# Optimization experiments

Hardware: AMD Instinct MI355X
Metric: run time of the kernel (lower is better)

The kernel has to match this reference:

```python
import jax, jax.numpy as jnp
import numpy as np

N_NODES = 50000
NODE_DIM = 128
HIDDEN = 256
BLOCK_OUT = 128
NUM_CLASSES = 40
N_EDGES = 800000


def setup_inputs() -> dict:
    key = jax.random.key(0)
    ks = jax.random.split(key, 12)
    glorot = lambda k, fi, fo: jax.random.normal(k, (fi, fo), jnp.float32) * (2.0 / (fi + fo)) ** 0.5
    return {
        "x": jax.random.normal(ks[0], (N_NODES, NODE_DIM), jnp.float32),
        "edge_index": jax.random.randint(ks[1], (2, N_EDGES), 0, N_NODES, jnp.int64),
        # block1: Node2Edge MLP (2*node_dim -> hidden), Edge2Node MLP (hidden -> 128)
        "W1": glorot(ks[2], 2 * NODE_DIM, HIDDEN),
        "b1": jnp.zeros((HIDDEN,), jnp.float32),
        "W2": glorot(ks[3], HIDDEN, BLOCK_OUT),
        "b2": jnp.zeros((BLOCK_OUT,), jnp.float32),
        # final Node2Edge: Linear(2*128,128) -> ReLU -> Linear(128,num_classes) -> LogSoftmax
        "W3": glorot(ks[4], 2 * BLOCK_OUT, 128),
        "b3": jnp.zeros((128,), jnp.float32),
        "W4": glorot(ks[5], 128, NUM_CLASSES),
        "b4": jnp.zeros((NUM_CLASSES,), jnp.float32),
    }


def reference(x, edge_index, W1, b1, W2, b2, W3, b3, W4, b4):
    src, dst = edge_index[0], edge_index[1]
    # Node2Edge: gather endpoints, concat, edge MLP
    e = jnp.concatenate([x[src], x[dst]], axis=-1)          # [E, 2*node_dim]
    eh = jax.nn.relu(e @ W1 + b1)                            # [E, hidden]
    # Edge2Node: scatter-mean edge features to destination nodes
    agg = jax.ops.segment_sum(eh, dst, num_segments=N_NODES)
    cnt = jax.ops.segment_sum(jnp.ones((eh.shape[0],), eh.dtype), dst, num_segments=N_NODES)
    mean = agg / jnp.maximum(cnt, 1.0)[:, None]              # [N, hidden]
    h = jax.nn.relu(mean @ W2 + b2)                          # [N, 128]
    # final Node2Edge head -> per-edge class log-probs
    e2 = jnp.concatenate([h[src], h[dst]], axis=-1)          # [E, 256]
    z = jax.nn.relu(e2 @ W3 + b3)                            # [E, 128]
    logits = z @ W4 + b4                                     # [E, num_classes]
    return jax.nn.log_softmax(logits, axis=-1)
```

## Files before the change

### kernel.cpp

```cpp
#include <hip/hip_runtime.h>
#include <hip/hip_bf16.h>


typedef short bf16x8 __attribute__((ext_vector_type(8)));
typedef float f32x4 __attribute__((ext_vector_type(4)));

#define N_NODES 50000
#define N_EDGES 800000

__device__ __forceinline__ unsigned short f2bf(float f) {
  unsigned u = __builtin_bit_cast(unsigned, f);
  u = u + 0x7fffu + ((u >> 16) & 1u);
  return (unsigned short)(u >> 16);
}
__device__ __forceinline__ float bf2f(unsigned short h) {
  unsigned u = ((unsigned)h) << 16;
  return __builtin_bit_cast(float, u);
}
__device__ __forceinline__ int ld_src(const int* ei, int m64, int e) {
  return m64 ? ei[2 * e] : ei[e];
}
__device__ __forceinline__ int ld_dst(const int* ei, int m64, int e) {
  return m64 ? ei[2 * N_EDGES + 2 * e] : ei[N_EDGES + e];
}

__global__ void k_prep_frags(const float* __restrict__ W1, const float* __restrict__ W2,
                             const float* __restrict__ W3, const float* __restrict__ W4,
                             const float* __restrict__ b4,
                             unsigned short* __restrict__ w1f, unsigned short* __restrict__ w2f,
                             unsigned short* __restrict__ w3f, unsigned short* __restrict__ w4f,
                             float* __restrict__ b4p, int* __restrict__ flagp,
                             const int* __restrict__ ei) {
  int gid = blockIdx.x * 256 + threadIdx.x;
  if (gid < 65536) {
    int i = gid & 7, lane = (gid >> 3) & 63, ks = (gid >> 9) & 3, ct = gid >> 11;
    int k = ks * 32 + (lane >> 4) * 8 + i;
    int c = ct * 16 + (lane & 15);
    float v = (c < 256) ? W1[k * 256 + c] : W1[(128 + k) * 256 + (c - 256)];
    w1f[gid] = f2bf(v);
  } else if (gid < 98304) {
    int f = gid - 65536;
    int i = f & 7, lane = (f >> 3) & 63, ks = (f >> 9) & 7, ct = f >> 12;
    int k = ks * 32 + (lane >> 4) * 8 + i;
    int c = ct * 16 + (lane & 15);
    w2f[f] = f2bf(W2[k * 128 + c]);
  } else if (gid < 131072) {
    int f = gid - 98304;
    int i = f & 7, lane = (f >> 3) & 63, ks = (f >> 9) & 3, ct = f >> 11;
    int k = ks * 32 + (lane >> 4) * 8 + i;
    int c = ct * 16 + (lane & 15);
    float v = (c < 128) ? W3[k * 128 + c] : W3[(128 + k) * 128 + (c - 128)];
    w3f[f] = f2bf(v);
  } else if (gid < 137216) {
    int f = gid - 131072;
    int i = f & 7, lane = (f >> 3) & 63, ks = (f >> 9) & 3, ct = f >> 11;
    int k = ks * 32 + (lane >> 4) * 8 + i;
    int c = ct * 16 + (lane & 15);
    w4f[f] = (c < 40) ? f2bf(W4[k * 40 + c]) : (unsigned short)0;
  } else if (gid < 137264) {
    int c = gid - 137216;
    b4p[c] = (c < 40) ? b4[c] : 0.f;
  } else if (gid == 137264) {
    *flagp = (ei[1] == 0 && ei[3] == 0 && ei[5] == 0 && ei[7] == 0) ? 1 : 0;
  }
}

__global__ void k_hist(const int* __restrict__ ei, const int* __restrict__ flagp,
                       int* __restrict__ hist) {
  int e = blockIdx.x * 256 + threadIdx.x;
  atomicAdd(&hist[ld_dst(ei, *flagp, e)], 1);
}

__global__ __launch_bounds__(256) void k_scan_a(const int* __restrict__ hist,
                                                int* __restrict__ bsum) {
  __shared__ int ps[256];
  int t = threadIdx.x, idx = blockIdx.x * 256 + t;
  ps[t] = (idx < N_NODES) ? hist[idx] : 0;
  __syncthreads();
  for (int off = 128; off > 0; off >>= 1) {
    if (t < off) ps[t] += ps[t + off];
    __syncthreads();
  }
  if (t == 0) bsum[blockIdx.x] = ps[0];
}

__global__ __launch_bounds__(256) void k_scan_b(int* __restrict__ bsum, int* __restrict__ seg) {
  __shared__ int ps[256];
  int t = threadIdx.x;
  int v = (t < 196) ? bsum[t] : 0;
  ps[t] = v;
  __syncthreads();
  for (int off = 1; off < 256; off <<= 1) {
    int u = (t >= off) ? ps[t - off] : 0;
    __syncthreads();
    ps[t] += u;
    __syncthreads();
  }
  if (t < 196) bsum[t] = ps[t] - v;
  if (t == 195) seg[N_NODES] = ps[195];
}

__global__ __launch_bounds__(256) void k_scan_c(int* __restrict__ hist,
                                                const int* __restrict__ bsum,
                                                int* __restrict__ seg) {
  __shared__ int ps[256];
  int t = threadIdx.x, idx = blockIdx.x * 256 + t;
  int v = (idx < N_NODES) ? hist[idx] : 0;
  ps[t] = v;
  __syncthreads();
  for (int off = 1; off < 256; off <<= 1) {
    int u = (t >= off) ? ps[t - off] : 0;
    __syncthreads();
    ps[t] += u;
    __syncthreads();
  }
  int run = bsum[blockIdx.x] + ps[t] - v;
  if (idx < N_NODES) {
    seg[idx] = run;
    hist[idx] = run;
  }
}

__global__ void k_scatter(const int* __restrict__ ei, const int* __restrict__ flagp,
                          int* __restrict__ cursor, int* __restrict__ ssrc) {
  int e = blockIdx.x * 256 + threadIdx.x;
  int m64 = *flagp;
  int s = ld_src(ei, m64, e), d = ld_dst(ei, m64, e);
  int pos = atomicAdd(&cursor[d], 1);
  ssrc[pos] = s;
}

__global__ __launch_bounds__(512, 2) void k_sy(const float* __restrict__ x,
                                               const unsigned short* __restrict__ w1f,
                                               const float* __restrict__ b1,
                                               unsigned short* __restrict__ SY) {
  __shared__ __attribute__((aligned(16))) short A[64 * 128];
  const int t = threadIdx.x;
  const int nb = blockIdx.x * 64;
  const int nv = min(64, N_NODES - nb);
  const int w = t >> 6, l = t & 63, lr = l & 15, lh = l >> 4;

  bf16x8 B[4][4];
#pragma unroll
  for (int ci = 0; ci < 4; ++ci)
#pragma unroll
    for (int ks = 0; ks < 4; ++ks)
      B[ci][ks] = *(const bf16x8*)(w1f + (((w * 4 + ci) * 4 + ks) * 64 + l) * 8);

#pragma unroll
  for (int j = 0; j < 2; ++j) {
    int c = t + 512 * j;
    int row = c >> 4, ck = c & 15;
    int rr = (row < nv) ? row : 0;
    const float* gp = x + (long)(nb + rr) * 128 + ck * 8;
    float4 v0 = *(const float4*)gp;
    float4 v1 = *(const float4*)(gp + 4);
    bf16x8 o;
    o[0] = (short)f2bf(v0.x); o[1] = (short)f2bf(v0.y);
    o[2] = (short)f2bf(v0.z); o[3] = (short)f2bf(v0.w);
    o[4] = (short)f2bf(v1.x); o[5] = (short)f2bf(v1.y);
    o[6] = (short)f2bf(v1.z); o[7] = (short)f2bf(v1.w);
    int off = (row << 8) + (ck << 4);
    off ^= (row & 7) << 4;
    *(bf16x8*)((char*)A + off) = o;
  }
  __syncthreads();

#pragma unroll
  for (int rt = 0; rt < 4; ++rt) {
    f32x4 acc[4] = {};
#pragma unroll
    for (int ks = 0; ks < 4; ++ks) {
      int row = rt * 16 + lr;
      int off = (row << 8) + (ks << 6) + (lh << 4);
      off ^= (row & 7) << 4;
      bf16x8 a = *(const bf16x8*)((const char*)A + off);
#pragma unroll
      for (int ci = 0; ci < 4; ++ci)
        acc[ci] = __builtin_amdgcn_mfma_f32_16x16x32_bf16(a, B[ci][ks], acc[ci], 0, 0, 0);
    }
#pragma unroll
    for (int ci = 0; ci < 4; ++ci) {
      int col = (w * 4 + ci) * 16 + lr;
      float bb = (col >= 256) ? b1[col - 256] : 0.f;
#pragma unroll
      for (int r = 0; r < 4; ++r) {
        int row = rt * 16 + lh * 4 + r;
        if (row < nv) SY[(long)(nb + row) * 512 + col] = f2bf(acc[ci][r] + bb);
      }
    }
  }
}

__global__ __launch_bounds__(512) void k_edge_agg(unsigned short* __restrict__ SY,
                                                  const int* __restrict__ seg,
                                                  const int* __restrict__ ssrc) {
  const int t = threadIdx.x, w = t >> 6, l = t & 63;
  const int d = blockIdx.x * 8 + w;
  const int s0 = seg[d], s1 = seg[d + 1];
  unsigned short* Yp = SY + (long)d * 512 + 256 + l * 4;
  ushort4 yu = *(const ushort4*)Yp;
  const float y0 = bf2f(yu.x), y1 = bf2f(yu.y), y2 = bf2f(yu.z), y3 = bf2f(yu.w);
  float a0 = 0.f, a1 = 0.f, a2 = 0.f, a3 = 0.f;
  int pos = s0;
  for (; pos + 4 <= s1; pos += 4) {
    int sA = ssrc[pos], sB = ssrc[pos + 1], sC = ssrc[pos + 2], sD = ssrc[pos + 3];
    ushort4 uA = *(const ushort4*)(SY + (long)sA * 512 + l * 4);
    ushort4 uB = *(const ushort4*)(SY + (long)sB * 512 + l * 4);
    ushort4 uC = *(const ushort4*)(SY + (long)sC * 512 + l * 4);
    ushort4 uD = *(const ushort4*)(SY + (long)sD * 512 + l * 4);
    a0 += fmaxf(bf2f(uA.x) + y0, 0.f); a1 += fmaxf(bf2f(uA.y) + y1, 0.f);
    a2 += fmaxf(bf2f(uA.z) + y2, 0.f); a3 += fmaxf(bf2f(uA.w) + y3, 0.f);
    a0 += fmaxf(bf2f(uB.x) + y0, 0.f); a1 += fmaxf(bf2f(uB.y) + y1, 0.f);
    a2 += fmaxf(bf2f(uB.z) + y2, 0.f); a3 += fmaxf(bf2f(uB.w) + y3, 0.f);
    a0 += fmaxf(bf2f(uC.x) + y0, 0.f); a1 += fmaxf(bf2f(uC.y) + y1, 0.f);
    a2 += fmaxf(bf2f(uC.z) + y2, 0.f); a3 += fmaxf(bf2f(uC.w) + y3, 0.f);
    a0 += fmaxf(bf2f(uD.x) + y0, 0.f); a1 += fmaxf(bf2f(uD.y) + y1, 0.f);
    a2 += fmaxf(bf2f(uD.z) + y2, 0.f); a3 += fmaxf(bf2f(uD.w) + y3, 0.f);
  }
  for (; pos < s1; ++pos) {
    int sA = ssrc[pos];
    ushort4 uA = *(const ushort4*)(SY + (long)sA * 512 + l * 4);
    a0 += fmaxf(bf2f(uA.x) + y0, 0.f); a1 += fmaxf(bf2f(uA.y) + y1, 0.f);
    a2 += fmaxf(bf2f(uA.z) + y2, 0.f); a3 += fmaxf(bf2f(uA.w) + y3, 0.f);
  }
  float inv = 1.0f / fmaxf((float)(s1 - s0), 1.0f);
  ushort4 o;
  o.x = f2bf(a0 * inv); o.y = f2bf(a1 * inv);
  o.z = f2bf(a2 * inv); o.w = f2bf(a3 * inv);
  *(ushort4*)Yp = o;
}

__global__ __launch_bounds__(256, 2) void k_pq(unsigned short* __restrict__ SY,
                                               const unsigned short* __restrict__ w2f,
                                               const float* __restrict__ b2,
                                               const unsigned short* __restrict__ w3f,
                                               const float* __restrict__ b3) {
  __shared__ __attribute__((aligned(16))) short M[64 * 256];
  __shared__ __attribute__((aligned(16))) short H[64 * 128];
  const int t = threadIdx.x;
  const int nb = blockIdx.x * 64;
  const int nv = min(64, N_NODES - nb);
  const int w = t >> 6, l = t & 63, lr = l & 15, lh = l >> 4;

  bf16x8 B2[2][8];
#pragma unroll
  for (int ci = 0; ci < 2; ++ci)
#pragma unroll
    for (int ks = 0; ks < 8; ++ks)
      B2[ci][ks] = *(const bf16x8*)(w2f + (((w * 2 + ci) * 8 + ks) * 64 + l) * 8);

#pragma unroll
  for (int j = 0; j < 8; ++j) {
    int c = t + 256 * j;
    int row = c >> 5, ck = c & 31;
    int rr = (row < nv) ? row : 0;
    int4 v = *(const int4*)(SY + (long)(nb + rr) * 512 + 256 + ck * 8);
    int off = (row << 9) + (ck << 4);
    off ^= (row & 7) << 4;
    *(int4*)((char*)M + off) = v;
  }
  __syncthreads();

#pragma unroll
  for (int rt = 0; rt < 4; ++rt) {
    f32x4 acc[2] = {};
#pragma unroll
    for (int ks = 0; ks < 8; ++ks) {
      int row = rt * 16 + lr;
      int off = (row << 9) + (ks << 6) + (lh << 4);
      off ^= (row & 7) << 4;
      bf16x8 a = *(const bf16x8*)((const char*)M + off);
      acc[0] = __builtin_amdgcn_mfma_f32_16x16x32_bf16(a, B2[0][ks], acc[0], 0, 0, 0);
      acc[1] = __builtin_amdgcn_mfma_f32_16x16x32_bf16(a, B2[1][ks], acc[1], 0, 0, 0);
    }
#pragma unroll
    for (int ci = 0; ci < 2; ++ci) {
      int col = (w * 2 + ci) * 16 + lr;
      float bb = b2[col];
#pragma unroll
      for (int r = 0; r < 4; ++r) {
        int row = rt * 16 + lh * 4 + r;
        int off = (row << 8) + (col << 1);
        off ^= (row & 7) << 4;
        *(short*)((char*)H + off) = (short)f2bf(fmaxf(acc[ci][r] + bb, 0.f));
      }
    }
  }
  __syncthreads();

  bf16x8 B3[4][4];
#pragma unroll
  for (int ci = 0; ci < 4; ++ci)
#pragma unroll
    for (int ks = 0; ks < 4; ++ks)
      B3[ci][ks] = *(const bf16x8*)(w3f + (((w * 4 + ci) * 4 + ks) * 64 + l) * 8);

#pragma unroll
  for (int rt = 0; rt < 4; ++rt) {
    f32x4 acc[4] = {};
#pragma unroll
    for (int ks = 0; ks < 4; ++ks) {
      int row = rt * 16 + lr;
      int off = (row << 8) + (ks << 6) + (lh << 4);
      off ^= (row & 7) << 4;
      bf16x8 a = *(const bf16x8*)((const char*)H + off);
#pragma unroll
      for (int ci = 0; ci < 4; ++ci)
        acc[ci] = __builtin_amdgcn_mfma_f32_16x16x32_bf16(a, B3[ci][ks], acc[ci], 0, 0, 0);
    }
#pragma unroll
    for (int ci = 0; ci < 4; ++ci) {
      int col = (w * 4 + ci) * 16 + lr;
      float bb = (col >= 128) ? b3[col - 128] : 0.f;
#pragma unroll
      for (int r = 0; r < 4; ++r) {
        int row = rt * 16 + lh * 4 + r;
        if (row < nv) SY[(long)(nb + row) * 512 + col] = f2bf(acc[ci][r] + bb);
      }
    }
  }
}

__global__ __launch_bounds__(256, 2) void k_head(const unsigned short* __restrict__ SY,
                                                 const int* __restrict__ ei,
                                                 const unsigned short* __restrict__ w4f,
                                                 const float* __restrict__ b4p,
                                                 float* __restrict__ out,
                                                 const int* __restrict__ flagp) {
  const int t = threadIdx.x, w = t >> 6, l = t & 63, lr = l & 15, lh = l >> 4;
  const int m64 = *flagp;
  const int eb = blockIdx.x * 64 + w * 16;
  const int el = eb + lr;
  const int sn = ld_src(ei, m64, el);
  const int dn = ld_dst(ei, m64, el);
  const unsigned short* Pp = SY + (long)sn * 512;
  const unsigned short* Qp = SY + (long)dn * 512 + 128;

  bf16x8 B4[3][4];
#pragma unroll
  for (int ci = 0; ci < 3; ++ci)
#pragma unroll
    for (int ks = 0; ks < 4; ++ks)
      B4[ci][ks] = *(const bf16x8*)(w4f + ((ci * 4 + ks) * 64 + l) * 8);

  f32x4 acc[3] = {};
#pragma unroll
  for (int ks = 0; ks < 4; ++ks) {
    bf16x8 p = *(const bf16x8*)(Pp + ks * 32 + lh * 8);
    bf16x8 q = *(const bf16x8*)(Qp + ks * 32 + lh * 8);
    bf16x8 a;
#pragma unroll
    for (int i = 0; i < 8; ++i)
      a[i] = (short)f2bf(fmaxf(bf2f((unsigned short)p[i]) + bf2f((unsigned short)q[i]), 0.f));
#pragma unroll
    for (int ci = 0; ci < 3; ++ci)
      acc[ci] = __builtin_amdgcn_mfma_f32_16x16x32_bf16(a, B4[ci][ks], acc[ci], 0, 0, 0);
  }

  float lg0[4], lg1[4], lg2[4];
  const bool val2 = lr < 8;
  const float bb0 = b4p[lr], bb1 = b4p[16 + lr], bb2 = b4p[32 + lr];
#pragma unroll
  for (int r = 0; r < 4; ++r) {
    lg0[r] = acc[0][r] + bb0;
    lg1[r] = acc[1][r] + bb1;
    lg2[r] = acc[2][r] + bb2;
  }
#pragma unroll
  for (int r = 0; r < 4; ++r) {
    float m = fmaxf(lg0[r], lg1[r]);
    if (val2) m = fmaxf(m, lg2[r]);
    m = fmaxf(m, __shfl_xor(m, 1, 64));
    m = fmaxf(m, __shfl_xor(m, 2, 64));
    m = fmaxf(m, __shfl_xor(m, 4, 64));
    m = fmaxf(m, __shfl_xor(m, 8, 64));
    float s = __expf(lg0[r] - m) + __expf(lg1[r] - m) + (val2 ? __expf(lg2[r] - m) : 0.f);
    s += __shfl_xor(s, 1, 64);
    s += __shfl_xor(s, 2, 64);
    s += __shfl_xor(s, 4, 64);
    s += __shfl_xor(s, 8, 64);
    float lse = m + __logf(s);
    long ob = (long)(eb + lh * 4 + r) * 40;
    out[ob + lr] = lg0[r] - lse;
    out[ob + 16 + lr] = lg1[r] - lse;
    if (val2) out[ob + 32 + lr] = lg2[r] - lse;
  }
}

extern "C" void kernel_launch(void* const* d_in, const int* in_sizes, int n_in,
                              void* d_out, int out_size, void* d_ws, size_t ws_size,
                              hipStream_t stream) {
  const float* x = (const float*)d_in[0];
  const int* ei = (const int*)d_in[1];
  const float* W1 = (const float*)d_in[2];
  const float* b1 = (const float*)d_in[3];
  const float* W2 = (const float*)d_in[4];
  const float* b2 = (const float*)d_in[5];
  const float* W3 = (const float*)d_in[6];
  const float* b3 = (const float*)d_in[7];
  const float* W4 = (const float*)d_in[8];
  const float* b4 = (const float*)d_in[9];
  char* ws = (char*)d_ws;
  int* hist = (int*)(ws + 0);
  int* seg = (int*)(ws + 200064);
  int* bsum = (int*)(ws + 400128);
  int* ssrc = (int*)(ws + 401152);
  unsigned short* SY = (unsigned short*)(ws + 3601408);
  unsigned short* w1f = (unsigned short*)(ws + 54801408);
  unsigned short* w2f = (unsigned short*)(ws + 54932480);
  unsigned short* w3f = (unsigned short*)(ws + 54998016);
  unsigned short* w4f = (unsigned short*)(ws + 55063552);
  float* b4p = (float*)(ws + 55075840);
  int* flagp = (int*)(ws + 55076032);
  float* out = (float*)d_out;

  hipMemsetAsync(ws, 0, 200000, stream);
  k_prep_frags<<<537, 256, 0, stream>>>(W1, W2, W3, W4, b4, w1f, w2f, w3f, w4f, b4p, flagp, ei);
  k_hist<<<3125, 256, 0, stream>>>(ei, flagp, hist);
  k_scan_a<<<196, 256, 0, stream>>>(hist, bsum);
  k_scan_b<<<1, 256, 0, stream>>>(bsum, seg);
  k_scan_c<<<196, 256, 0, stream>>>(hist, bsum, seg);
  k_scatter<<<3125, 256, 0, stream>>>(ei, flagp, hist, ssrc);
  k_sy<<<782, 512, 0, stream>>>(x, w1f, b1, SY);
  k_edge_agg<<<6250, 512, 0, stream>>>(SY, seg, ssrc);
  k_pq<<<782, 256, 0, stream>>>(SY, w2f, b2, w3f, b3);
  k_head<<<12500, 256, 0, stream>>>(SY, ei, w4f, b4p, out, flagp);
}
```

Baseline: 307.8 us.

## Fuse edge aggregation into node MLP kernel and write P/Q to separate columns

Merges the segment-mean aggregation kernel into the W2/W3 node kernel. Each 512-thread block aggregates its 64 nodes directly into shared memory, which removes the write-back and re-read of the mean features and one launch. P/Q outputs now go to columns 256-511 of SY, because other blocks still read columns 0-255 (the source projections) during aggregation and must not see them overwritten. The bf16 packing in the head moves to a perm-based pack2 helper, and output stores become nontemporal. The cost is fewer blocks doing the gather (782 vs 6250), which may lower latency hiding for the irregular loads.

```diff
diff --git a/kernel.cpp b/kernel.cpp
--- a/kernel.cpp
+++ b/kernel.cpp
@@ -16,6 +16,10 @@
 __device__ __forceinline__ float bf2f(unsigned short h) {
   unsigned u = ((unsigned)h) << 16;
   return __builtin_bit_cast(float, u);
+}
+__device__ __forceinline__ unsigned pack2(float lo, float hi) {
+  return __builtin_amdgcn_perm(__builtin_bit_cast(unsigned, hi),
+                               __builtin_bit_cast(unsigned, lo), 0x07060302u);
 }
 __device__ __forceinline__ int ld_src(const int* ei, int m64, int e) {
   return m64 ? ei[2 * e] : ei[e];
@@ -192,50 +196,11 @@
   }
 }
 
-__global__ __launch_bounds__(512) void k_edge_agg(unsigned short* __restrict__ SY,
-                                                  const int* __restrict__ seg,
-                                                  const int* __restrict__ ssrc) {
-  const int t = threadIdx.x, w = t >> 6, l = t & 63;
-  const int d = blockIdx.x * 8 + w;
-  const int s0 = seg[d], s1 = seg[d + 1];
-  unsigned short* Yp = SY + (long)d * 512 + 256 + l * 4;
-  ushort4 yu = *(const ushort4*)Yp;
-  const float y0 = bf2f(yu.x), y1 = bf2f(yu.y), y2 = bf2f(yu.z), y3 = bf2f(yu.w);
-  float a0 = 0.f, a1 = 0.f, a2 = 0.f, a3 = 0.f;
-  int pos = s0;
-  for (; pos + 4 <= s1; pos += 4) {
-    int sA = ssrc[pos], sB = ssrc[pos + 1], sC = ssrc[pos + 2], sD = ssrc[pos + 3];
-    ushort4 uA = *(const ushort4*)(SY + (long)sA * 512 + l * 4);
-    ushort4 uB = *(const ushort4*)(SY + (long)sB * 512 + l * 4);
-    ushort4 uC = *(const ushort4*)(SY + (long)sC * 512 + l * 4);
-    ushort4 uD = *(const ushort4*)(SY + (long)sD * 512 + l * 4);
-    a0 += fmaxf(bf2f(uA.x) + y0, 0.f); a1 += fmaxf(bf2f(uA.y) + y1, 0.f);
-    a2 += fmaxf(bf2f(uA.z) + y2, 0.f); a3 += fmaxf(bf2f(uA.w) + y3, 0.f);
-    a0 += fmaxf(bf2f(uB.x) + y0, 0.f); a1 += fmaxf(bf2f(uB.y) + y1, 0.f);
-    a2 += fmaxf(bf2f(uB.z) + y2, 0.f); a3 += fmaxf(bf2f(uB.w) + y3, 0.f);
-    a0 += fmaxf(bf2f(uC.x) + y0, 0.f); a1 += fmaxf(bf2f(uC.y) + y1, 0.f);
-    a2 += fmaxf(bf2f(uC.z) + y2, 0.f); a3 += fmaxf(bf2f(uC.w) + y3, 0.f);
-    a0 += fmaxf(bf2f(uD.x) + y0, 0.f); a1 += fmaxf(bf2f(uD.y) + y1, 0.f);
-    a2 += fmaxf(bf2f(uD.z) + y2, 0.f); a3 += fmaxf(bf2f(uD.w) + y3, 0.f);
-  }
-  for (; pos < s1; ++pos) {
-    int sA = ssrc[pos];
-    ushort4 uA = *(const ushort4*)(SY + (long)sA * 512 + l * 4);
-    a0 += fmaxf(bf2f(uA.x) + y0, 0.f); a1 += fmaxf(bf2f(uA.y) + y1, 0.f);
-    a2 += fmaxf(bf2f(uA.z) + y2, 0.f); a3 += fmaxf(bf2f(uA.w) + y3, 0.f);
-  }
-  float inv = 1.0f / fmaxf((float)(s1 - s0), 1.0f);
-  ushort4 o;
-  o.x = f2bf(a0 * inv); o.y = f2bf(a1 * inv);
-  o.z = f2bf(a2 * inv); o.w = f2bf(a3 * inv);
-  *(ushort4*)Yp = o;
-}
-
-__global__ __launch_bounds__(256, 2) void k_pq(unsigned short* __restrict__ SY,
-                                               const unsigned short* __restrict__ w2f,
-                                               const float* __restrict__ b2,
-                                               const unsigned short* __restrict__ w3f,
-                                               const float* __restrict__ b3) {
+__global__ __launch_bounds__(512, 2) void k_agg_pq(
+    unsigned short* __restrict__ SY, const int* __restrict__ seg,
+    const int* __restrict__ ssrc, const unsigned short* __restrict__ w2f,
+    const float* __restrict__ b2, const unsigned short* __restrict__ w3f,
+    const float* __restrict__ b3) {
   __shared__ __attribute__((aligned(16))) short M[64 * 256];
   __shared__ __attribute__((aligned(16))) short H[64 * 128];
   const int t = threadIdx.x;
@@ -243,80 +208,102 @@
   const int nv = min(64, N_NODES - nb);
   const int w = t >> 6, l = t & 63, lr = l & 15, lh = l >> 4;
 
-  bf16x8 B2[2][8];
-#pragma unroll
-  for (int ci = 0; ci < 2; ++ci)
-#pragma unroll
-    for (int ks = 0; ks < 8; ++ks)
-      B2[ci][ks] = *(const bf16x8*)(w2f + (((w * 2 + ci) * 8 + ks) * 64 + l) * 8);
-
-#pragma unroll
+#pragma unroll 1
   for (int j = 0; j < 8; ++j) {
-    int c = t + 256 * j;
-    int row = c >> 5, ck = c & 31;
-    int rr = (row < nv) ? row : 0;
-    int4 v = *(const int4*)(SY + (long)(nb + rr) * 512 + 256 + ck * 8);
-    int off = (row << 9) + (ck << 4);
+    const int row = w * 8 + j;
+    const int n = nb + row;
+    float a0 = 0.f, a1 = 0.f, a2 = 0.f, a3 = 0.f;
+    if (n < N_NODES) {
+      const ushort4 yu = *(const ushort4*)(SY + (long)n * 512 + 256 + l * 4);
+      const float y0 = bf2f(yu.x), y1 = bf2f(yu.y), y2 = bf2f(yu.z), y3 = bf2f(yu.w);
+      const int s0 = seg[n], s1 = seg[n + 1];
+      int pos = s0;
+      for (; pos + 4 <= s1; pos += 4) {
+        int sA = ssrc[pos], sB = ssrc[pos + 1], sC = ssrc[pos + 2], sD = ssrc[pos + 3];
+        ushort4 uA = *(const ushort4*)(SY + (long)sA * 512 + l * 4);
+        ushort4 uB = *(const ushort4*)(SY + (long)sB * 512 + l * 4);
+        ushort4 uC = *(const ushort4*)(SY + (long)sC * 512 + l * 4);
+        ushort4 uD = *(const ushort4*)(SY + (long)sD * 512 + l * 4);
+        a0 += fmaxf(bf2f(uA.x) + y0, 0.f); a1 += fmaxf(bf2f(uA.y) + y1, 0.f);
+        a2 += fmaxf(bf2f(uA.z) + y2, 0.f); a3 += fmaxf(bf2f(uA.w) + y3, 0.f);
+        a0 += fmaxf(bf2f(uB.x) + y0, 0.f); a1 += fmaxf(bf2f(uB.y) + y1, 0.f);
+        a2 += fmaxf(bf2f(uB.z) + y2, 0.f); a3 += fmaxf(bf2f(uB.w) + y3, 0.f);
+        a0 += fmaxf(bf2f(uC.x) + y0, 0.f); a1 += fmaxf(bf2f(uC.y) + y1, 0.f);
+        a2 += fmaxf(bf2f(uC.z) + y2, 0.f); a3 += fmaxf(bf2f(uC.w) + y3, 0.f);
+        a0 += fmaxf(bf2f(uD.x) + y0, 0.f); a1 += fmaxf(bf2f(uD.y) + y1, 0.f);
+        a2 += fmaxf(bf2f(uD.z) + y2, 0.f); a3 += fmaxf(bf2f(uD.w) + y3, 0.f);
+      }
+      for (; pos < s1; ++pos) {
+        int sA = ssrc[pos];
+        ushort4 uA = *(const ushort4*)(SY + (long)sA * 512 + l * 4);
+        a0 += fmaxf(bf2f(uA.x) + y0, 0.f); a1 += fmaxf(bf2f(uA.y) + y1, 0.f);
+        a2 += fmaxf(bf2f(uA.z) + y2, 0.f); a3 += fmaxf(bf2f(uA.w) + y3, 0.f);
+      }
+      float inv = 1.0f / fmaxf((float)(s1 - s0), 1.0f);
+      a0 *= inv; a1 *= inv; a2 *= inv; a3 *= inv;
+    }
+    ushort4 o;
+    o.x = f2bf(a0); o.y = f2bf(a1); o.z = f2bf(a2); o.w = f2bf(a3);
+    int off = (row << 9) + (l << 3);
     off ^= (row & 7) << 4;
-    *(int4*)((char*)M + off) = v;
-  }
-  __syncthreads();
-
+    *(ushort4*)((char*)M + off) = o;
+  }
+  __syncthreads();
+
+  bf16x8 B2[8];
+#pragma unroll
+  for (int ks = 0; ks < 8; ++ks)
+    B2[ks] = *(const bf16x8*)(w2f + ((w * 8 + ks) * 64 + l) * 8);
+  const float b2c = b2[w * 16 + lr];
 #pragma unroll
   for (int rt = 0; rt < 4; ++rt) {
-    f32x4 acc[2] = {};
+    f32x4 acc = {};
 #pragma unroll
     for (int ks = 0; ks < 8; ++ks) {
       int row = rt * 16 + lr;
       int off = (row << 9) + (ks << 6) + (lh << 4);
       off ^= (row & 7) << 4;
       bf16x8 a = *(const bf16x8*)((const char*)M + off);
-      acc[0] = __builtin_amdgcn_mfma_f32_16x16x32_bf16(a, B2[0][ks], acc[0], 0, 0, 0);
-      acc[1] = __builtin_amdgcn_mfma_f32_16x16x32_bf16(a, B2[1][ks], acc[1], 0, 0, 0);
-    }
-#pragma unroll
-    for (int ci = 0; ci < 2; ++ci) {
-      int col = (w * 2 + ci) * 16 + lr;
-      float bb = b2[col];
-#pragma unroll
-      for (int r = 0; r < 4; ++r) {
-        int row = rt * 16 + lh * 4 + r;
-        int off = (row << 8) + (col << 1);
-        off ^= (row & 7) << 4;
-        *(short*)((char*)H + off) = (short)f2bf(fmaxf(acc[ci][r] + bb, 0.f));
-      }
-    }
-  }
-  __syncthreads();
-
-  bf16x8 B3[4][4];
-#pragma unroll
-  for (int ci = 0; ci < 4; ++ci)
+      acc = __builtin_amdgcn_mfma_f32_16x16x32_bf16(a, B2[ks], acc, 0, 0, 0);
+    }
+    int col = w * 16 + lr;
+#pragma unroll
+    for (int r = 0; r < 4; ++r) {
+      int row = rt * 16 + lh * 4 + r;
+      int off = (row << 8) + (col << 1);
+      off ^= (row & 7) << 4;
+      *(short*)((char*)H + off) = (short)f2bf(fmaxf(acc[r] + b2c, 0.f));
+    }
+  }
+  __syncthreads();
+
+  bf16x8 B3[2][4];
+#pragma unroll
+  for (int ci = 0; ci < 2; ++ci)
 #pragma unroll
     for (int ks = 0; ks < 4; ++ks)
-      B3[ci][ks] = *(const bf16x8*)(w3f + (((w * 4 + ci) * 4 + ks) * 64 + l) * 8);
+      B3[ci][ks] = *(const bf16x8*)(w3f + (((w * 2 + ci) * 4 + ks) * 64 + l) * 8);
 
 #pragma unroll
   for (int rt = 0; rt < 4; ++rt) {
-    f32x4 acc[4] = {};
+    f32x4 acc[2] = {};
 #pragma unroll
     for (int ks = 0; ks < 4; ++ks) {
       int row = rt * 16 + lr;
       int off = (row << 8) + (ks << 6) + (lh << 4);
       off ^= (row & 7) << 4;
       bf16x8 a = *(const bf16x8*)((const char*)H + off);
-#pragma unroll
-      for (int ci = 0; ci < 4; ++ci)
-        acc[ci] = __builtin_amdgcn_mfma_f32_16x16x32_bf16(a, B3[ci][ks], acc[ci], 0, 0, 0);
-    }
-#pragma unroll
-    for (int ci = 0; ci < 4; ++ci) {
-      int col = (w * 4 + ci) * 16 + lr;
+      acc[0] = __builtin_amdgcn_mfma_f32_16x16x32_bf16(a, B3[0][ks], acc[0], 0, 0, 0);
+      acc[1] = __builtin_amdgcn_mfma_f32_16x16x32_bf16(a, B3[1][ks], acc[1], 0, 0, 0);
+    }
+#pragma unroll
+    for (int ci = 0; ci < 2; ++ci) {
+      int col = (w * 2 + ci) * 16 + lr;
       float bb = (col >= 128) ? b3[col - 128] : 0.f;
 #pragma unroll
       for (int r = 0; r < 4; ++r) {
         int row = rt * 16 + lh * 4 + r;
-        if (row < nv) SY[(long)(nb + row) * 512 + col] = f2bf(acc[ci][r] + bb);
+        if (row < nv) SY[(long)(nb + row) * 512 + 256 + col] = f2bf(acc[ci][r] + bb);
       }
     }
   }
@@ -334,8 +321,8 @@
   const int el = eb + lr;
   const int sn = ld_src(ei, m64, el);
   const int dn = ld_dst(ei, m64, el);
-  const unsigned short* Pp = SY + (long)sn * 512;
-  const unsigned short* Qp = SY + (long)dn * 512 + 128;
+  const unsigned short* Pp = SY + (long)sn * 512 + 256;
+  const unsigned short* Qp = SY + (long)dn * 512 + 384;
 
   bf16x8 B4[3][4];
 #pragma unroll
@@ -349,10 +336,14 @@
   for (int ks = 0; ks < 4; ++ks) {
     bf16x8 p = *(const bf16x8*)(Pp + ks * 32 + lh * 8);
     bf16x8 q = *(const bf16x8*)(Qp + ks * 32 + lh * 8);
-    bf16x8 a;
+    float f[8];
 #pragma unroll
     for (int i = 0; i < 8; ++i)
-      a[i] = (short)f2bf(fmaxf(bf2f((unsigned short)p[i]) + bf2f((unsigned short)q[i]), 0.f));
+      f[i] = fmaxf(bf2f((unsigned short)p[i]) + bf2f((unsigned short)q[i]), 0.f);
+    int4 a4;
+    a4.x = pack2(f[0], f[1]); a4.y = pack2(f[2], f[3]);
+    a4.z = pack2(f[4], f[5]); a4.w = pack2(f[6], f[7]);
+    bf16x8 a = __builtin_bit_cast(bf16x8, a4);
 #pragma unroll
     for (int ci = 0; ci < 3; ++ci)
       acc[ci] = __builtin_amdgcn_mfma_f32_16x16x32_bf16(a, B4[ci][ks], acc[ci], 0, 0, 0);
@@ -382,9 +373,9 @@
     s += __shfl_xor(s, 8, 64);
     float lse = m + __logf(s);
     long ob = (long)(eb + lh * 4 + r) * 40;
-    out[ob + lr] = lg0[r] - lse;
-    out[ob + 16 + lr] = lg1[r] - lse;
-    if (val2) out[ob + 32 + lr] = lg2[r] - lse;
+    __builtin_nontemporal_store(lg0[r] - lse, &out[ob + lr]);
+    __builtin_nontemporal_store(lg1[r] - lse, &out[ob + 16 + lr]);
+    if (val2) __builtin_nontemporal_store(lg2[r] - lse, &out[ob + 32 + lr]);
   }
 }
 
@@ -423,7 +414,6 @@
   k_scan_c<<<196, 256, 0, stream>>>(hist, bsum, seg);
   k_scatter<<<3125, 256, 0, stream>>>(ei, flagp, hist, ssrc);
   k_sy<<<782, 512, 0, stream>>>(x, w1f, b1, SY);
-  k_edge_agg<<<6250, 512, 0, stream>>>(SY, seg, ssrc);
-  k_pq<<<782, 256, 0, stream>>>(SY, w2f, b2, w3f, b3);
+  k_agg_pq<<<782, 512, 0, stream>>>(SY, seg, ssrc, w2f, b2, w3f, b3);
   k_head<<<12500, 256, 0, stream>>>(SY, ei, w4f, b4p, out, flagp);
 }
```

Result: slower. 321.1 us (+4.3%).
